# Optimization experiments

Hardware: AMD Instinct MI355X
Metric: run time of the kernel (lower is better)

The kernel has to match this reference:

```python
import jax, jax.numpy as jnp
import numpy as np

B, S, HID = 2, 2048, 1024
H = 16
D = HID // H  # 64
SCALE = 1.0 / float(np.sqrt(D))


def setup_inputs() -> dict:
    key = jax.random.key(0)
    ks = jax.random.split(key, 12)
    s = 0.02
    return {
        "query": jax.random.normal(ks[0], (B, S, HID), jnp.float32),
        "key": jax.random.normal(ks[1], (B, S, HID), jnp.float32),
        "value": jax.random.normal(ks[2], (B, S, HID), jnp.float32),
        "attention_mask": jnp.ones((B, S, S), jnp.int32),
        "Wq": jax.random.normal(ks[3], (HID, HID), jnp.float32) * s,
        "bq": jnp.zeros((HID,), jnp.float32),
        "Wk": jax.random.normal(ks[4], (HID, HID), jnp.float32) * s,
        "bk": jnp.zeros((HID,), jnp.float32),
        "Wv": jax.random.normal(ks[5], (HID, HID), jnp.float32) * s,
        "bv": jnp.zeros((HID,), jnp.float32),
        "Wo": jax.random.normal(ks[6], (HID, HID), jnp.float32) * s,
        "bo": jnp.zeros((HID,), jnp.float32),
    }


def _split_heads(x):  # [B,S,HID] -> [B,H,S,D]
    b, s, _ = x.shape
    return x.reshape(b, s, H, D).transpose(0, 2, 1, 3)


def reference(query, key, value, attention_mask, Wq, bq, Wk, bk, Wv, bv, Wo, bo):
    # Projections (torch Linear: x @ W.T + b)
    Q = _split_heads(query @ Wq.T + bq)
    K = _split_heads(key @ Wk.T + bk)
    V = _split_heads(value @ Wv.T + bv)
    # Full attention; chunking in the original is math-equivalent (softmax over full key axis per chunk)
    scores = jnp.einsum("bhqd,bhkd->bhqk", Q, K) * SCALE
    scores = jnp.where(attention_mask[:, None, :, :] == 0, jnp.float32(-1e9), scores)
    attn = jax.nn.softmax(scores, axis=-1)  # dropout is identity in eval mode
    ctx = jnp.einsum("bhqk,bhkd->bhqd", attn, V)
    ctx = ctx.transpose(0, 2, 1, 3).reshape(query.shape[0], query.shape[1], HID)
    out = ctx @ Wo.T + bo
    # module returns a dummy uniform attention-weight tensor
    attn_weights = jnp.full((query.shape[0], H, S, S), 1.0 / S, dtype=query.dtype)
    return (out, attn_weights)
```

## Files before the change

### kernel.cpp

```cpp
#include <hip/hip_runtime.h>

typedef float f4v __attribute__((ext_vector_type(4)));
typedef float f8v __attribute__((ext_vector_type(8)));
typedef short s4v __attribute__((ext_vector_type(4)));
typedef short s8v __attribute__((ext_vector_type(8)));
typedef __bf16 bf4t __attribute__((ext_vector_type(4)));
typedef __bf16 bf8t __attribute__((ext_vector_type(8)));
typedef unsigned short u16;
typedef unsigned int u32;

#define S_LEN 2048
#define HIDN 1024
#define NH 16
#define HD 64
#define QS 0.180336879f
#define DTH 11.5415603f
#define FILLV 0.00048828125f

__device__ __forceinline__ u16 f2bf(float f) {
  return __builtin_bit_cast(u16, (__bf16)f);
}

__device__ __forceinline__ s8v cvt8(f4v x, f4v y) {
  const f8v f = {x[0], x[1], x[2], x[3], y[0], y[1], y[2], y[3]};
  return __builtin_bit_cast(s8v, __builtin_convertvector(f, bf8t));
}

__device__ __forceinline__ s4v cvt4(f4v x) {
  return __builtin_bit_cast(s4v, __builtin_convertvector(x, bf4t));
}

__device__ __forceinline__ f4v mfma16(s8v a, s8v b, f4v c) {
  return __builtin_amdgcn_mfma_f32_16x16x32_bf16(
      __builtin_bit_cast(bf8t, a), __builtin_bit_cast(bf8t, b), c, 0, 0, 0);
}

__device__ __forceinline__ void gl16(const void* g, void* l) {
  __builtin_amdgcn_global_load_lds((const __attribute__((address_space(1))) u32*)g,
                                   (__attribute__((address_space(3))) u32*)l, 16, 0, 0);
}

#define FILL_DECL(nblk)                                        \
  const f4v fvv = (f4v){FILLV, FILLV, FILLV, FILLV};           \
  f4v* fp = fillb + (size_t)bid * 256 + threadIdx.x;           \
  f4v* const fpe = fillb + fill4;                               \
  const size_t FT = (size_t)(nblk) * 256;

#define FILL_STORE()                                           \
  do { if (fp < fpe) __builtin_nontemporal_store(fvv, fp);     \
       fp += FT; } while (0)

struct PrepArgs { const float* w[4]; u16* d[4]; const int* mask; unsigned* pm; unsigned* flg; };

__global__ __launch_bounds__(256) void prep(PrepArgs a) {
  const int y = blockIdx.y;
  const int tid = threadIdx.x;
  if (y < 4) {
    const float* s = a.w[y];
    u16* d = a.d[y];
#pragma unroll
    for (int j = 0; j < 2; ++j) {
      const int i = blockIdx.x * 256 + tid + j * 65536;
      const f4v x0 = ((const f4v*)s)[2 * i];
      const f4v x1 = ((const f4v*)s)[2 * i + 1];
      ((s8v*)d)[i] = cvt8(x0, x1);
    }
  } else {
    const int lane = tid & 63;
    const size_t base = (size_t)(y - 4) * 2097152;
    bool anyz = false;
    for (int j = 0; j < 32; ++j) {
      const size_t i = base + (size_t)blockIdx.x * 256 + tid + (size_t)j * 65536;
      const unsigned long long bb = __ballot(a.mask[i] != 0);
      if (lane == 0) a.pm[i >> 5] = (unsigned)bb;
      if (lane == 32) a.pm[i >> 5] = (unsigned)(bb >> 32);
      anyz |= (bb != ~0ull);
    }
    if (anyz && lane == 0) a.flg[0] = 1u;
  }
}

struct QkvArgs {
  const float* A[3]; const u16* W[3]; const float* bias[3]; u16* out[3];
  f4v* fillb; size_t fill4;
};

__global__ __launch_bounds__(256) void gemm_qkv(QkvArgs ga) {
  __shared__ __align__(16) u16 As[128 * 32];
  __shared__ __align__(16) u16 Bs[128 * 32];
  const int p = blockIdx.x;
  const int xcd = p & 7;
  const int ii = p >> 3;
  const int ytile = xcd * 12 + (ii >> 3);
  const int xt = ii & 7;
  const int id = ytile >> 5;
  const int tid = threadIdx.x;
  const int lane = tid & 63;
  const int wv = tid >> 6;
  const int wm = wv >> 1, wn = wv & 1;
  const int g = lane >> 4, l15 = lane & 15;
  const int m0 = (ytile & 31) * 128, n0 = xt * 128;
  const int bid = p;
  f4v* fillb = ga.fillb;
  const size_t fill4 = ga.fill4;
  FILL_DECL(768);

  f4v acc[4][4];
#pragma unroll
  for (int i = 0; i < 4; ++i)
#pragma unroll
    for (int j = 0; j < 4; ++j) acc[i][j] = (f4v){0.f, 0.f, 0.f, 0.f};

  const int ar = tid >> 1;
  const int ac = (tid & 1) * 16;
  const float* ap = ga.A[id] + (size_t)(m0 + ar) * HIDN + ac;
  const u16* bp0 = ga.W[id] + (size_t)(n0 + (tid >> 2)) * HIDN + (tid & 3) * 8;
  const u16* bp1 = bp0 + (size_t)64 * HIDN;
  u16* bsl0 = Bs + tid * 8;
  u16* bsl1 = Bs + 2048 + tid * 8;
  u16* asl = As + ar * 32 + ac;

  for (int kt = 0; kt < HIDN; kt += 32) {
    const f4v a0 = ((const f4v*)(ap + kt))[0];
    const f4v a1 = ((const f4v*)(ap + kt))[1];
    const f4v a2 = ((const f4v*)(ap + kt))[2];
    const f4v a3 = ((const f4v*)(ap + kt))[3];
    __syncthreads();
    gl16(bp0 + kt, bsl0);
    gl16(bp1 + kt, bsl1);
    *(s8v*)asl = cvt8(a0, a1);
    *(s8v*)(asl + 8) = cvt8(a2, a3);
    __syncthreads();
    FILL_STORE();
    FILL_STORE();
    s8v af[4], bfv[4];
#pragma unroll
    for (int i = 0; i < 4; ++i)
      af[i] = *(const s8v*)(As + (wm * 64 + i * 16 + l15) * 32 + g * 8);
#pragma unroll
    for (int j = 0; j < 4; ++j)
      bfv[j] = *(const s8v*)(Bs + (wn * 64 + j * 16 + l15) * 32 + g * 8);
#pragma unroll
    for (int i = 0; i < 4; ++i)
#pragma unroll
      for (int j = 0; j < 4; ++j) acc[i][j] = mfma16(af[i], bfv[j], acc[i][j]);
  }

  const float* bias = ga.bias[id];
  u16* out = ga.out[id];
  const int mode2 = (id == 2);
  const float osc = (id == 0) ? QS : 1.0f;
#pragma unroll
  for (int i = 0; i < 4; ++i) {
#pragma unroll
    for (int j = 0; j < 4; ++j) {
      const int mb = m0 + wm * 64 + i * 16 + g * 4;
      const int n = n0 + wn * 64 + j * 16 + l15;
      const float bv = bias[n];
#pragma unroll
      for (int r = 0; r < 4; ++r) {
        const int m = mb + r;
        const float v = (acc[i][j][r] + bv) * osc;
        const int b = m >> 11, s = m & 2047, h = n >> 6, d = n & 63;
        if (mode2) {
          out[((size_t)(b * NH + h) * HD + d) * S_LEN + s] = f2bf(v);
        } else {
          out[(((size_t)(b * NH + h) * S_LEN + s) << 6) + d] = f2bf(v);
        }
      }
    }
  }
}

__global__ __launch_bounds__(256) void attn_fused(
    const u16* __restrict__ Qb, const u16* __restrict__ Kb,
    const u16* __restrict__ Vtb, u16* __restrict__ ctxb,
    const unsigned* __restrict__ pm, const unsigned* __restrict__ flg,
    f4v* __restrict__ fillb, const size_t fill4) {
  __shared__ __align__(16) u16 Ks[64 * 64];
  __shared__ __align__(16) u16 Vs[64 * 64];
  __shared__ __align__(16) u16 Ps[4][16 * 64];
  __shared__ unsigned mw[64][2];

  const int p = blockIdx.x;
  const int xcd = p & 7;
  const int ii = p >> 3;
  const int bh = xcd * 4 + (ii >> 5);
  const int q0 = (ii & 31) * 64;
  const int tid = threadIdx.x;
  const int lane = tid & 63;
  const int wv = tid >> 6;
  const int g = lane >> 4, l15 = lane & 15;
  const int b = bh >> 4, h = bh & 15;
  const bool allones = (flg[0] == 0u);
  const int bid = p;
  FILL_DECL(1024);

  const u16* qp = Qb + ((size_t)bh * S_LEN + q0 + wv * 16 + l15) * HD + g * 8;
  const s8v qb0 = *(const s8v*)qp;
  const s8v qb1 = *(const s8v*)(qp + 32);

  f4v o[4];
#pragma unroll
  for (int nb = 0; nb < 4; ++nb) o[nb] = (f4v){0.f, 0.f, 0.f, 0.f};
  float mr = -INFINITY, lr = 0.f;

  const int sr = tid >> 3;
  const int sg = tid & 7;
  const int sc0 = ((sg ^ (sr & 7)) * 8);
  const u16* kp0 = Kb + ((size_t)bh * S_LEN + sr) * HD + sc0;
  const u16* kp1 = kp0 + (size_t)32 * HD;
  const u16* vp0 = Vtb + ((size_t)bh * HD + sr) * S_LEN + sc0;
  const u16* vp1 = vp0 + (size_t)32 * S_LEN;
  u16* kl = Ks + tid * 8;
  u16* vl = Vs + tid * 8;
  u16* pw = Ps[wv];

  for (int kt = 0; kt < S_LEN; kt += 64) {
    __syncthreads();
    gl16(kp0 + (size_t)kt * HD, kl);
    gl16(kp1 + (size_t)kt * HD, kl + 2048);
    gl16(vp0 + kt, vl);
    gl16(vp1 + kt, vl + 2048);
    if (!allones && tid < 128) {
      mw[tid >> 1][tid & 1] =
          pm[((size_t)b * S_LEN + q0 + (tid >> 1)) * (S_LEN / 32) + (kt >> 5) + (tid & 1)];
    }
    __syncthreads();
    FILL_STORE();
    FILL_STORE();

    f4v sc[4];
    __builtin_amdgcn_s_setprio(1);
#pragma unroll
    for (int nb = 0; nb < 4; ++nb) {
      const int kr = nb * 16 + l15;
      const s8v ka0 = *(const s8v*)(Ks + kr * 64 + ((g ^ (kr & 7)) * 8));
      const s8v ka1 = *(const s8v*)(Ks + kr * 64 + (((4 + g) ^ (kr & 7)) * 8));
      f4v z = (f4v){0.f, 0.f, 0.f, 0.f};
      z = mfma16(ka0, qb0, z);
      z = mfma16(ka1, qb1, z);
      sc[nb] = z;
    }
    __builtin_amdgcn_s_setprio(0);
    if (!allones) {
      const int qr = wv * 16 + l15;
      const unsigned w0 = mw[qr][0], w1 = mw[qr][1];
#pragma unroll
      for (int nb = 0; nb < 4; ++nb) {
        const unsigned wmk = (nb < 2) ? w0 : w1;
#pragma unroll
        for (int r = 0; r < 4; ++r) {
          const int bit = ((nb & 1) << 4) + (g << 2) + r;
          if (!((wmk >> bit) & 1u)) sc[nb][r] = -1e9f;
        }
      }
    }

    float tm = sc[0][0];
#pragma unroll
    for (int nb = 0; nb < 4; ++nb)
#pragma unroll
      for (int r = 0; r < 4; ++r) tm = fmaxf(tm, sc[nb][r]);
    tm = fmaxf(tm, __shfl_xor(tm, 16, 64));
    tm = fmaxf(tm, __shfl_xor(tm, 32, 64));
    if (!__all(tm <= mr + DTH)) {
      const float mn = fmaxf(mr, tm);
      const float al = exp2f(mr - mn);
      mr = mn;
      lr *= al;
#pragma unroll
      for (int r = 0; r < 4; ++r) {
        const float ar = __shfl(al, (g << 2) + r, 64);
#pragma unroll
        for (int nb = 0; nb < 4; ++nb) o[nb][r] *= ar;
      }
    }
    float rs = 0.f;
#pragma unroll
    for (int nb = 0; nb < 4; ++nb)
#pragma unroll
      for (int r = 0; r < 4; ++r) {
        const float p_ = exp2f(sc[nb][r] - mr);
        sc[nb][r] = p_;
        rs += p_;
      }
    rs += __shfl_xor(rs, 16, 64);
    rs += __shfl_xor(rs, 32, 64);
    lr += rs;
#pragma unroll
    for (int nb = 0; nb < 4; ++nb) {
      *(s4v*)(pw + l15 * 64 + ((nb * 16 + g * 4) ^ ((l15 & 7) * 8))) = cvt4(sc[nb]);
    }

    const s8v pa0 = *(const s8v*)(pw + l15 * 64 + ((g ^ (l15 & 7)) * 8));
    const s8v pa1 = *(const s8v*)(pw + l15 * 64 + (((4 + g) ^ (l15 & 7)) * 8));

    __builtin_amdgcn_s_setprio(1);
#pragma unroll
    for (int nb = 0; nb < 4; ++nb) {
      const int vr = nb * 16 + l15;
      const s8v vb0 = *(const s8v*)(Vs + vr * 64 + ((g ^ (vr & 7)) * 8));
      const s8v vb1 = *(const s8v*)(Vs + vr * 64 + (((4 + g) ^ (vr & 7)) * 8));
      o[nb] = mfma16(pa0, vb0, o[nb]);
      o[nb] = mfma16(pa1, vb1, o[nb]);
    }
    __builtin_amdgcn_s_setprio(0);
  }

#pragma unroll
  for (int r = 0; r < 4; ++r) {
    const float linv = 1.f / __shfl(lr, (g << 2) + r, 64);
    const int q = q0 + wv * 16 + g * 4 + r;
#pragma unroll
    for (int nb = 0; nb < 4; ++nb) {
      const int d = nb * 16 + l15;
      ctxb[(((size_t)b * S_LEN + q) * NH + h) * HD + d] = f2bf(o[nb][r] * linv);
    }
  }
}

__global__ __launch_bounds__(256) void gemm_out(
    const u16* __restrict__ A, const u16* __restrict__ W,
    const float* __restrict__ bias, float* __restrict__ out,
    f4v* __restrict__ fillb, const size_t fill4) {
  __shared__ __align__(16) u16 As[128 * 32];
  __shared__ __align__(16) u16 Bs[64 * 32];
  const int p = blockIdx.x;
  const int xcd = p & 7;
  const int ii = p >> 3;
  const int m0 = (xcd * 4 + (ii >> 4)) * 128;
  const int n0 = (ii & 15) * 64;
  const int tid = threadIdx.x;
  const int lane = tid & 63;
  const int wv = tid >> 6;
  const int wm = wv >> 1, wn = wv & 1;
  const int g = lane >> 4, l15 = lane & 15;
  const int bid = p;
  FILL_DECL(512);

  f4v acc[4][2];
#pragma unroll
  for (int i = 0; i < 4; ++i)
#pragma unroll
    for (int j = 0; j < 2; ++j) acc[i][j] = (f4v){0.f, 0.f, 0.f, 0.f};

  const u16* ap0 = A + (size_t)(m0 + (tid >> 2)) * HIDN + (tid & 3) * 8;
  const u16* ap1 = ap0 + (size_t)64 * HIDN;
  const u16* bp0 = W + (size_t)(n0 + (tid >> 2)) * HIDN + (tid & 3) * 8;
  u16* asl0 = As + tid * 8;
  u16* asl1 = As + 2048 + tid * 8;
  u16* bsl0 = Bs + tid * 8;

  for (int kt = 0; kt < HIDN; kt += 32) {
    __syncthreads();
    gl16(ap0 + kt, asl0);
    gl16(ap1 + kt, asl1);
    gl16(bp0 + kt, bsl0);
    __syncthreads();
    FILL_STORE();
    s8v af[4], bfv[2];
#pragma unroll
    for (int i = 0; i < 4; ++i)
      af[i] = *(const s8v*)(As + (wm * 64 + i * 16 + l15) * 32 + g * 8);
#pragma unroll
    for (int j = 0; j < 2; ++j)
      bfv[j] = *(const s8v*)(Bs + (wn * 32 + j * 16 + l15) * 32 + g * 8);
#pragma unroll
    for (int i = 0; i < 4; ++i)
#pragma unroll
      for (int j = 0; j < 2; ++j) acc[i][j] = mfma16(af[i], bfv[j], acc[i][j]);
  }

#pragma unroll
  for (int i = 0; i < 4; ++i) {
#pragma unroll
    for (int j = 0; j < 2; ++j) {
      const int mb = m0 + wm * 64 + i * 16 + g * 4;
      const int n = n0 + wn * 32 + j * 16 + l15;
      const float bv = bias[n];
#pragma unroll
      for (int r = 0; r < 4; ++r) {
        out[(size_t)(mb + r) * HIDN + n] = acc[i][j][r] + bv;
      }
    }
  }
}

__global__ void fill_tail(float* __restrict__ p, const size_t n4) {
  const f4v v = (f4v){FILLV, FILLV, FILLV, FILLV};
  size_t i = (size_t)blockIdx.x * blockDim.x + threadIdx.x;
  const size_t st = (size_t)gridDim.x * blockDim.x;
  f4v* p4 = (f4v*)p;
  for (; i < n4; i += st) p4[i] = v;
}

extern "C" void kernel_launch(void* const* d_in, const int* in_sizes, int n_in,
                              void* d_out, int out_size, void* d_ws, size_t ws_size,
                              hipStream_t stream) {
  const float* query = (const float*)d_in[0];
  const float* key_ = (const float*)d_in[1];
  const float* value = (const float*)d_in[2];
  const int* amask = (const int*)d_in[3];
  const float* Wq = (const float*)d_in[4];
  const float* bq = (const float*)d_in[5];
  const float* Wk = (const float*)d_in[6];
  const float* bk = (const float*)d_in[7];
  const float* Wv = (const float*)d_in[8];
  const float* bv = (const float*)d_in[9];
  const float* Wo = (const float*)d_in[10];
  const float* bo = (const float*)d_in[11];

  float* out = (float*)d_out;
  const size_t OUT0 = (size_t)2 * S_LEN * HIDN;
  float* outw = out + OUT0;

  const size_t MB = (size_t)1 << 20;
  const size_t CARVE = 48 * MB;
  const bool use_ws = ws_size >= CARVE;
  char* scratch = use_ws ? (char*)d_ws : (char*)outw;

  u16* wq16 = (u16*)(scratch);
  u16* wk16 = (u16*)(scratch + 2 * MB);
  u16* wv16 = (u16*)(scratch + 4 * MB);
  u16* wo16 = (u16*)(scratch + 6 * MB);
  u16* Qb = (u16*)(scratch + 8 * MB);
  u16* Kb = (u16*)(scratch + 16 * MB);
  u16* Vtb = (u16*)(scratch + 24 * MB);
  u16* ctxb = (u16*)(scratch + 32 * MB);
  unsigned* pm = (unsigned*)(scratch + 40 * MB);
  unsigned* flg = (unsigned*)(scratch + 41 * MB);

  f4v* fillp;
  size_t F;
  if (use_ws) {
    fillp = (f4v*)outw;
    F = 33554432;
  } else {
    fillp = (f4v*)(outw + CARVE / 4);
    F = 33554432 - CARVE / 16;
  }
  const size_t capq = (size_t)768 * 256 * 64;
  const size_t capa = (size_t)1024 * 256 * 64;
  const size_t cq = F < capq ? F : capq;
  const size_t F1 = F - cq;
  const size_t ca = F1 < capa ? F1 : capa;
  const size_t co = F1 - ca;
  f4v* fq = fillp;
  f4v* fa = fq + cq;
  f4v* fo = fa + ca;

  hipMemsetAsync(flg, 0, 4, stream);

  PrepArgs pa;
  pa.w[0] = Wq; pa.w[1] = Wk; pa.w[2] = Wv; pa.w[3] = Wo;
  pa.d[0] = wq16; pa.d[1] = wk16; pa.d[2] = wv16; pa.d[3] = wo16;
  pa.mask = amask; pa.pm = pm; pa.flg = flg;
  prep<<<dim3(256, 8), 256, 0, stream>>>(pa);

  QkvArgs qa;
  qa.A[0] = query; qa.A[1] = key_; qa.A[2] = value;
  qa.W[0] = wq16; qa.W[1] = wk16; qa.W[2] = wv16;
  qa.bias[0] = bq; qa.bias[1] = bk; qa.bias[2] = bv;
  qa.out[0] = Qb; qa.out[1] = Kb; qa.out[2] = Vtb;
  qa.fillb = fq; qa.fill4 = cq;
  gemm_qkv<<<768, 256, 0, stream>>>(qa);

  attn_fused<<<1024, 256, 0, stream>>>(Qb, Kb, Vtb, ctxb, pm, flg, fa, ca);

  gemm_out<<<512, 256, 0, stream>>>(ctxb, wo16, bo, out, fo, co);

  if (!use_ws) {
    fill_tail<<<2048, 256, 0, stream>>>(outw, CARVE / 16);
  }
}
```

Before: 194.9 us.

## Double K-depth per iteration in GEMMs and attention, shuffle P in registers

Both GEMMs now stage a 64-deep K slice per barrier pair instead of 32, with XOR-swizzled LDS layouts to avoid bank conflicts. The attention kernel loads 128 keys per iteration and processes them in two halves, which halves the barrier count. It also converts the P tile to the MFMA A-operand layout with cross-lane shuffles instead of an LDS round trip. The uniform attn_weights fill is rebalanced across kernels, with part of it moved into the prep kernel. Larger LDS tiles and the occupancy hints in launch_bounds may reduce or constrain occupancy.

```diff
diff --git a/kernel.cpp b/kernel.cpp
--- a/kernel.cpp
+++ b/kernel.cpp
@@ -8,6 +8,7 @@
 typedef __bf16 bf8t __attribute__((ext_vector_type(8)));
 typedef unsigned short u16;
 typedef unsigned int u32;
+typedef unsigned long long u64;
 
 #define S_LEN 2048
 #define HIDN 1024
@@ -50,11 +51,18 @@
   do { if (fp < fpe) __builtin_nontemporal_store(fvv, fp);     \
        fp += FT; } while (0)
 
-struct PrepArgs { const float* w[4]; u16* d[4]; const int* mask; unsigned* pm; unsigned* flg; };
+struct PrepArgs {
+  const float* w[4]; u16* d[4]; const int* mask; unsigned* pm; unsigned* flg;
+  f4v* fillb; size_t fill4;
+};
 
 __global__ __launch_bounds__(256) void prep(PrepArgs a) {
   const int y = blockIdx.y;
   const int tid = threadIdx.x;
+  const int bid = y * 256 + blockIdx.x;
+  f4v* fillb = a.fillb;
+  const size_t fill4 = a.fill4;
+  FILL_DECL(2048);
   if (y < 4) {
     const float* s = a.w[y];
     u16* d = a.d[y];
@@ -78,6 +86,8 @@
     }
     if (anyz && lane == 0) a.flg[0] = 1u;
   }
+#pragma unroll
+  for (int f = 0; f < 8; ++f) FILL_STORE();
 }
 
 struct QkvArgs {
@@ -85,9 +95,9 @@
   f4v* fillb; size_t fill4;
 };
 
-__global__ __launch_bounds__(256) void gemm_qkv(QkvArgs ga) {
-  __shared__ __align__(16) u16 As[128 * 32];
-  __shared__ __align__(16) u16 Bs[128 * 32];
+__global__ __launch_bounds__(256, 3) void gemm_qkv(QkvArgs ga) {
+  __shared__ __align__(16) u16 As[128 * 64];
+  __shared__ __align__(16) u16 Bs[128 * 64];
   const int p = blockIdx.x;
   const int xcd = p & 7;
   const int ii = p >> 3;
@@ -112,38 +122,51 @@
     for (int j = 0; j < 4; ++j) acc[i][j] = (f4v){0.f, 0.f, 0.f, 0.f};
 
   const int ar = tid >> 1;
-  const int ac = (tid & 1) * 16;
-  const float* ap = ga.A[id] + (size_t)(m0 + ar) * HIDN + ac;
-  const u16* bp0 = ga.W[id] + (size_t)(n0 + (tid >> 2)) * HIDN + (tid & 3) * 8;
-  const u16* bp1 = bp0 + (size_t)64 * HIDN;
-  u16* bsl0 = Bs + tid * 8;
-  u16* bsl1 = Bs + 2048 + tid * 8;
-  u16* asl = As + ar * 32 + ac;
-
-  for (int kt = 0; kt < HIDN; kt += 32) {
+  const int alc = (tid & 1) * 32;
+  const float* ap = ga.A[id] + (size_t)(m0 + ar) * HIDN + alc;
+  u16* asl = As + ar * 64;
+  const int sw_a = (ar & 7) * 8;
+  const int br = tid >> 3;
+  const u16* bp = ga.W[id] + (size_t)(n0 + br) * HIDN + (((tid & 7) ^ (br & 7)) * 8);
+  u16* bsl = Bs + tid * 8;
+  const int swf = (l15 & 7) * 8;
+
+  for (int kt = 0; kt < HIDN; kt += 64) {
     const f4v a0 = ((const f4v*)(ap + kt))[0];
     const f4v a1 = ((const f4v*)(ap + kt))[1];
     const f4v a2 = ((const f4v*)(ap + kt))[2];
     const f4v a3 = ((const f4v*)(ap + kt))[3];
+    const f4v a4 = ((const f4v*)(ap + kt))[4];
+    const f4v a5 = ((const f4v*)(ap + kt))[5];
+    const f4v a6 = ((const f4v*)(ap + kt))[6];
+    const f4v a7 = ((const f4v*)(ap + kt))[7];
     __syncthreads();
-    gl16(bp0 + kt, bsl0);
-    gl16(bp1 + kt, bsl1);
-    *(s8v*)asl = cvt8(a0, a1);
-    *(s8v*)(asl + 8) = cvt8(a2, a3);
+    gl16(bp + kt, bsl);
+    gl16(bp + kt + 32 * HIDN, bsl + 2048);
+    gl16(bp + kt + 64 * HIDN, bsl + 4096);
+    gl16(bp + kt + 96 * HIDN, bsl + 6144);
+    *(s8v*)(asl + ((alc + 0) ^ sw_a)) = cvt8(a0, a1);
+    *(s8v*)(asl + ((alc + 8) ^ sw_a)) = cvt8(a2, a3);
+    *(s8v*)(asl + ((alc + 16) ^ sw_a)) = cvt8(a4, a5);
+    *(s8v*)(asl + ((alc + 24) ^ sw_a)) = cvt8(a6, a7);
     __syncthreads();
     FILL_STORE();
     FILL_STORE();
-    s8v af[4], bfv[4];
-#pragma unroll
-    for (int i = 0; i < 4; ++i)
-      af[i] = *(const s8v*)(As + (wm * 64 + i * 16 + l15) * 32 + g * 8);
-#pragma unroll
-    for (int j = 0; j < 4; ++j)
-      bfv[j] = *(const s8v*)(Bs + (wn * 64 + j * 16 + l15) * 32 + g * 8);
-#pragma unroll
-    for (int i = 0; i < 4; ++i)
-#pragma unroll
-      for (int j = 0; j < 4; ++j) acc[i][j] = mfma16(af[i], bfv[j], acc[i][j]);
+#pragma unroll
+    for (int kk = 0; kk < 2; ++kk) {
+      const int fc = (kk * 32 + g * 8) ^ swf;
+      s8v af[4], bfv[4];
+#pragma unroll
+      for (int i = 0; i < 4; ++i)
+        af[i] = *(const s8v*)(As + (wm * 64 + i * 16 + l15) * 64 + fc);
+#pragma unroll
+      for (int j = 0; j < 4; ++j)
+        bfv[j] = *(const s8v*)(Bs + (wn * 64 + j * 16 + l15) * 64 + fc);
+#pragma unroll
+      for (int i = 0; i < 4; ++i)
+#pragma unroll
+        for (int j = 0; j < 4; ++j) acc[i][j] = mfma16(af[i], bfv[j], acc[i][j]);
+    }
   }
 
   const float* bias = ga.bias[id];
@@ -172,15 +195,14 @@
   }
 }
 
-__global__ __launch_bounds__(256) void attn_fused(
+__global__ __launch_bounds__(256, 4) void attn_fused(
     const u16* __restrict__ Qb, const u16* __restrict__ Kb,
     const u16* __restrict__ Vtb, u16* __restrict__ ctxb,
     const unsigned* __restrict__ pm, const unsigned* __restrict__ flg,
     f4v* __restrict__ fillb, const size_t fill4) {
-  __shared__ __align__(16) u16 Ks[64 * 64];
-  __shared__ __align__(16) u16 Vs[64 * 64];
-  __shared__ __align__(16) u16 Ps[4][16 * 64];
-  __shared__ unsigned mw[64][2];
+  __shared__ __align__(16) u16 Ks[2 * 64 * 64];
+  __shared__ __align__(16) u16 Vs[2 * 64 * 64];
+  __shared__ unsigned mw[64][4];
 
   const int p = blockIdx.x;
   const int xcd = p & 7;
@@ -206,106 +228,131 @@
   float mr = -INFINITY, lr = 0.f;
 
   const int sr = tid >> 3;
-  const int sg = tid & 7;
-  const int sc0 = ((sg ^ (sr & 7)) * 8);
-  const u16* kp0 = Kb + ((size_t)bh * S_LEN + sr) * HD + sc0;
-  const u16* kp1 = kp0 + (size_t)32 * HD;
-  const u16* vp0 = Vtb + ((size_t)bh * HD + sr) * S_LEN + sc0;
-  const u16* vp1 = vp0 + (size_t)32 * S_LEN;
+  const int sc0 = (((tid & 7) ^ (sr & 7)) * 8);
+  const u16* kp = Kb + ((size_t)bh * S_LEN + sr) * HD + sc0;
+  const u16* vp = Vtb + ((size_t)bh * HD + sr) * S_LEN + sc0;
   u16* kl = Ks + tid * 8;
   u16* vl = Vs + tid * 8;
-  u16* pw = Ps[wv];
-
-  for (int kt = 0; kt < S_LEN; kt += 64) {
+  const int srcA = ((g & 1) * 2) * 16 + l15;
+  const int srcB = srcA + 16;
+  const bool ghi = (g & 2) != 0;
+
+  for (int kt = 0; kt < S_LEN; kt += 128) {
     __syncthreads();
-    gl16(kp0 + (size_t)kt * HD, kl);
-    gl16(kp1 + (size_t)kt * HD, kl + 2048);
-    gl16(vp0 + kt, vl);
-    gl16(vp1 + kt, vl + 2048);
-    if (!allones && tid < 128) {
-      mw[tid >> 1][tid & 1] =
-          pm[((size_t)b * S_LEN + q0 + (tid >> 1)) * (S_LEN / 32) + (kt >> 5) + (tid & 1)];
+    const u16* kq = kp + (size_t)kt * HD;
+    gl16(kq, kl);
+    gl16(kq + 32 * HD, kl + 2048);
+    gl16(kq + 64 * HD, kl + 4096);
+    gl16(kq + 96 * HD, kl + 6144);
+    gl16(vp + kt, vl);
+    gl16(vp + 32 * S_LEN + kt, vl + 2048);
+    gl16(vp + kt + 64, vl + 4096);
+    gl16(vp + 32 * S_LEN + kt + 64, vl + 6144);
+    if (!allones) {
+      mw[tid >> 2][tid & 3] =
+          pm[((size_t)b * S_LEN + q0 + (tid >> 2)) * (S_LEN / 32) + (kt >> 5) + (tid & 3)];
     }
     __syncthreads();
     FILL_STORE();
     FILL_STORE();
-
-    f4v sc[4];
-    __builtin_amdgcn_s_setprio(1);
-#pragma unroll
-    for (int nb = 0; nb < 4; ++nb) {
-      const int kr = nb * 16 + l15;
-      const s8v ka0 = *(const s8v*)(Ks + kr * 64 + ((g ^ (kr & 7)) * 8));
-      const s8v ka1 = *(const s8v*)(Ks + kr * 64 + (((4 + g) ^ (kr & 7)) * 8));
-      f4v z = (f4v){0.f, 0.f, 0.f, 0.f};
-      z = mfma16(ka0, qb0, z);
-      z = mfma16(ka1, qb1, z);
-      sc[nb] = z;
-    }
-    __builtin_amdgcn_s_setprio(0);
-    if (!allones) {
-      const int qr = wv * 16 + l15;
-      const unsigned w0 = mw[qr][0], w1 = mw[qr][1];
+    FILL_STORE();
+    FILL_STORE();
+    FILL_STORE();
+
+#pragma unroll
+    for (int h2 = 0; h2 < 2; ++h2) {
+      const u16* Kh = Ks + h2 * 4096;
+      const u16* Vh = Vs + h2 * 4096;
+
+      f4v sc[4];
+      __builtin_amdgcn_s_setprio(1);
 #pragma unroll
       for (int nb = 0; nb < 4; ++nb) {
-        const unsigned wmk = (nb < 2) ? w0 : w1;
-#pragma unroll
-        for (int r = 0; r < 4; ++r) {
-          const int bit = ((nb & 1) << 4) + (g << 2) + r;
-          if (!((wmk >> bit) & 1u)) sc[nb][r] = -1e9f;
+        const int kr = nb * 16 + l15;
+        const s8v ka0 = *(const s8v*)(Kh + kr * 64 + ((g ^ (kr & 7)) * 8));
+        const s8v ka1 = *(const s8v*)(Kh + kr * 64 + (((4 + g) ^ (kr & 7)) * 8));
+        f4v z = (f4v){0.f, 0.f, 0.f, 0.f};
+        z = mfma16(ka0, qb0, z);
+        z = mfma16(ka1, qb1, z);
+        sc[nb] = z;
+      }
+      __builtin_amdgcn_s_setprio(0);
+      if (!allones) {
+        const int qr = wv * 16 + l15;
+        const unsigned w0 = mw[qr][h2 * 2], w1 = mw[qr][h2 * 2 + 1];
+#pragma unroll
+        for (int nb = 0; nb < 4; ++nb) {
+          const unsigned wmk = (nb < 2) ? w0 : w1;
+#pragma unroll
+          for (int r = 0; r < 4; ++r) {
+            const int bit = ((nb & 1) << 4) + (g << 2) + r;
+            if (!((wmk >> bit) & 1u)) sc[nb][r] = -1e9f;
+          }
         }
       }
-    }
-
-    float tm = sc[0][0];
-#pragma unroll
-    for (int nb = 0; nb < 4; ++nb)
-#pragma unroll
-      for (int r = 0; r < 4; ++r) tm = fmaxf(tm, sc[nb][r]);
-    tm = fmaxf(tm, __shfl_xor(tm, 16, 64));
-    tm = fmaxf(tm, __shfl_xor(tm, 32, 64));
-    if (!__all(tm <= mr + DTH)) {
-      const float mn = fmaxf(mr, tm);
-      const float al = exp2f(mr - mn);
-      mr = mn;
-      lr *= al;
-#pragma unroll
-      for (int r = 0; r < 4; ++r) {
-        const float ar = __shfl(al, (g << 2) + r, 64);
-#pragma unroll
-        for (int nb = 0; nb < 4; ++nb) o[nb][r] *= ar;
+
+      float tm = sc[0][0];
+#pragma unroll
+      for (int nb = 0; nb < 4; ++nb)
+#pragma unroll
+        for (int r = 0; r < 4; ++r) tm = fmaxf(tm, sc[nb][r]);
+      tm = fmaxf(tm, __shfl_xor(tm, 16, 64));
+      tm = fmaxf(tm, __shfl_xor(tm, 32, 64));
+      if (!__all(tm <= mr + DTH)) {
+        const float mn = fmaxf(mr, tm);
+        const float al = exp2f(mr - mn);
+        mr = mn;
+        lr *= al;
+#pragma unroll
+        for (int r = 0; r < 4; ++r) {
+          const float ar = __shfl(al, (g << 2) + r, 64);
+#pragma unroll
+          for (int nb = 0; nb < 4; ++nb) o[nb][r] *= ar;
+        }
       }
-    }
-    float rs = 0.f;
-#pragma unroll
-    for (int nb = 0; nb < 4; ++nb)
-#pragma unroll
-      for (int r = 0; r < 4; ++r) {
-        const float p_ = exp2f(sc[nb][r] - mr);
-        sc[nb][r] = p_;
-        rs += p_;
+      float rs = 0.f;
+#pragma unroll
+      for (int nb = 0; nb < 4; ++nb)
+#pragma unroll
+        for (int r = 0; r < 4; ++r) {
+          const float p_ = exp2f(sc[nb][r] - mr);
+          sc[nb][r] = p_;
+          rs += p_;
+        }
+      rs += __shfl_xor(rs, 16, 64);
+      rs += __shfl_xor(rs, 32, 64);
+      lr += rs;
+
+      const u64 c0 = __builtin_bit_cast(u64, cvt4(sc[0]));
+      const u64 c1 = __builtin_bit_cast(u64, cvt4(sc[1]));
+      const u64 c2 = __builtin_bit_cast(u64, cvt4(sc[2]));
+      const u64 c3 = __builtin_bit_cast(u64, cvt4(sc[3]));
+      const u64 a0A = __shfl(c0, srcA, 64);
+      const u64 a1A = __shfl(c1, srcA, 64);
+      const u64 a0B = __shfl(c0, srcB, 64);
+      const u64 a1B = __shfl(c1, srcB, 64);
+      const u64 a2A = __shfl(c2, srcA, 64);
+      const u64 a3A = __shfl(c3, srcA, 64);
+      const u64 a2B = __shfl(c2, srcB, 64);
+      const u64 a3B = __shfl(c3, srcB, 64);
+      const s4v lo0 = __builtin_bit_cast(s4v, ghi ? a1A : a0A);
+      const s4v hi0 = __builtin_bit_cast(s4v, ghi ? a1B : a0B);
+      const s4v lo1 = __builtin_bit_cast(s4v, ghi ? a3A : a2A);
+      const s4v hi1 = __builtin_bit_cast(s4v, ghi ? a3B : a2B);
+      const s8v pa0 = {lo0[0], lo0[1], lo0[2], lo0[3], hi0[0], hi0[1], hi0[2], hi0[3]};
+      const s8v pa1 = {lo1[0], lo1[1], lo1[2], lo1[3], hi1[0], hi1[1], hi1[2], hi1[3]};
+
+      __builtin_amdgcn_s_setprio(1);
+#pragma unroll
+      for (int nb = 0; nb < 4; ++nb) {
+        const int vr = nb * 16 + l15;
+        const s8v vb0 = *(const s8v*)(Vh + vr * 64 + ((g ^ (vr & 7)) * 8));
+        const s8v vb1 = *(const s8v*)(Vh + vr * 64 + (((4 + g) ^ (vr & 7)) * 8));
+        o[nb] = mfma16(pa0, vb0, o[nb]);
+        o[nb] = mfma16(pa1, vb1, o[nb]);
       }
-    rs += __shfl_xor(rs, 16, 64);
-    rs += __shfl_xor(rs, 32, 64);
-    lr += rs;
-#pragma unroll
-    for (int nb = 0; nb < 4; ++nb) {
-      *(s4v*)(pw + l15 * 64 + ((nb * 16 + g * 4) ^ ((l15 & 7) * 8))) = cvt4(sc[nb]);
-    }
-
-    const s8v pa0 = *(const s8v*)(pw + l15 * 64 + ((g ^ (l15 & 7)) * 8));
-    const s8v pa1 = *(const s8v*)(pw + l15 * 64 + (((4 + g) ^ (l15 & 7)) * 8));
-
-    __builtin_amdgcn_s_setprio(1);
-#pragma unroll
-    for (int nb = 0; nb < 4; ++nb) {
-      const int vr = nb * 16 + l15;
-      const s8v vb0 = *(const s8v*)(Vs + vr * 64 + ((g ^ (vr & 7)) * 8));
-      const s8v vb1 = *(const s8v*)(Vs + vr * 64 + (((4 + g) ^ (vr & 7)) * 8));
-      o[nb] = mfma16(pa0, vb0, o[nb]);
-      o[nb] = mfma16(pa1, vb1, o[nb]);
-    }
-    __builtin_amdgcn_s_setprio(0);
+      __builtin_amdgcn_s_setprio(0);
+    }
   }
 
 #pragma unroll
@@ -324,8 +371,8 @@
     const u16* __restrict__ A, const u16* __restrict__ W,
     const float* __restrict__ bias, float* __restrict__ out,
     f4v* __restrict__ fillb, const size_t fill4) {
-  __shared__ __align__(16) u16 As[128 * 32];
-  __shared__ __align__(16) u16 Bs[64 * 32];
+  __shared__ __align__(16) u16 As[128 * 64];
+  __shared__ __align__(16) u16 Bs[64 * 64];
   const int p = blockIdx.x;
   const int xcd = p & 7;
   const int ii = p >> 3;
@@ -345,31 +392,40 @@
 #pragma unroll
     for (int j = 0; j < 2; ++j) acc[i][j] = (f4v){0.f, 0.f, 0.f, 0.f};
 
-  const u16* ap0 = A + (size_t)(m0 + (tid >> 2)) * HIDN + (tid & 3) * 8;
-  const u16* ap1 = ap0 + (size_t)64 * HIDN;
-  const u16* bp0 = W + (size_t)(n0 + (tid >> 2)) * HIDN + (tid & 3) * 8;
-  u16* asl0 = As + tid * 8;
-  u16* asl1 = As + 2048 + tid * 8;
-  u16* bsl0 = Bs + tid * 8;
-
-  for (int kt = 0; kt < HIDN; kt += 32) {
+  const int br = tid >> 3;
+  const int scol = ((tid & 7) ^ (br & 7)) * 8;
+  const u16* ap = A + (size_t)(m0 + br) * HIDN + scol;
+  const u16* bp = W + (size_t)(n0 + br) * HIDN + scol;
+  u16* asl = As + tid * 8;
+  u16* bsl = Bs + tid * 8;
+  const int swf = (l15 & 7) * 8;
+
+  for (int kt = 0; kt < HIDN; kt += 64) {
     __syncthreads();
-    gl16(ap0 + kt, asl0);
-    gl16(ap1 + kt, asl1);
-    gl16(bp0 + kt, bsl0);
+    gl16(ap + kt, asl);
+    gl16(ap + kt + 32 * HIDN, asl + 2048);
+    gl16(ap + kt + 64 * HIDN, asl + 4096);
+    gl16(ap + kt + 96 * HIDN, asl + 6144);
+    gl16(bp + kt, bsl);
+    gl16(bp + kt + 32 * HIDN, bsl + 2048);
     __syncthreads();
     FILL_STORE();
-    s8v af[4], bfv[2];
-#pragma unroll
-    for (int i = 0; i < 4; ++i)
-      af[i] = *(const s8v*)(As + (wm * 64 + i * 16 + l15) * 32 + g * 8);
-#pragma unroll
-    for (int j = 0; j < 2; ++j)
-      bfv[j] = *(const s8v*)(Bs + (wn * 32 + j * 16 + l15) * 32 + g * 8);
-#pragma unroll
-    for (int i = 0; i < 4; ++i)
-#pragma unroll
-      for (int j = 0; j < 2; ++j) acc[i][j] = mfma16(af[i], bfv[j], acc[i][j]);
+    FILL_STORE();
+#pragma unroll
+    for (int kk = 0; kk < 2; ++kk) {
+      const int fc = (kk * 32 + g * 8) ^ swf;
+      s8v af[4], bfv[2];
+#pragma unroll
+      for (int i = 0; i < 4; ++i)
+        af[i] = *(const s8v*)(As + (wm * 64 + i * 16 + l15) * 64 + fc);
+#pragma unroll
+      for (int j = 0; j < 2; ++j)
+        bfv[j] = *(const s8v*)(Bs + (wn * 32 + j * 16 + l15) * 64 + fc);
+#pragma unroll
+      for (int i = 0; i < 4; ++i)
+#pragma unroll
+        for (int j = 0; j < 2; ++j) acc[i][j] = mfma16(af[i], bfv[j], acc[i][j]);
+    }
   }
 
 #pragma unroll
@@ -440,13 +496,16 @@
     fillp = (f4v*)(outw + CARVE / 4);
     F = 33554432 - CARVE / 16;
   }
-  const size_t capq = (size_t)768 * 256 * 64;
-  const size_t capa = (size_t)1024 * 256 * 64;
-  const size_t cq = F < capq ? F : capq;
-  const size_t F1 = F - cq;
-  const size_t ca = F1 < capa ? F1 : capa;
-  const size_t co = F1 - ca;
-  f4v* fq = fillp;
+  const size_t cap_p = (size_t)2048 * 256 * 8;
+  const size_t cap_q = (size_t)768 * 256 * 32;
+  const size_t cap_a = (size_t)1024 * 256 * 80;
+  size_t rem = F;
+  const size_t cp = rem < cap_p ? rem : cap_p; rem -= cp;
+  const size_t cq = rem < cap_q ? rem : cap_q; rem -= cq;
+  const size_t ca = rem < cap_a ? rem : cap_a; rem -= ca;
+  const size_t co = rem;
+  f4v* fP = fillp;
+  f4v* fq = fP + cp;
   f4v* fa = fq + cq;
   f4v* fo = fa + ca;
 
@@ -456,6 +515,7 @@
   pa.w[0] = Wq; pa.w[1] = Wk; pa.w[2] = Wv; pa.w[3] = Wo;
   pa.d[0] = wq16; pa.d[1] = wk16; pa.d[2] = wv16; pa.d[3] = wo16;
   pa.mask = amask; pa.pm = pm; pa.flg = flg;
+  pa.fillb = fP; pa.fill4 = cp;
   prep<<<dim3(256, 8), 256, 0, stream>>>(pa);
 
   QkvArgs qa;
```

New measurement: 217.0 us. 11.4% more time.
